# Optimization experiments

Hardware: AMD Instinct MI355X
Metric: run time of the kernel (lower is better)

Reference implementation:

```python
import jax, jax.numpy as jnp
import numpy as np

NUM_OBJ = 3
MIN_OBJ_SCALE = 0.1
MAX_OBJ_SCALE = 0.8
MIN_Y_SCALE = 0.75
MAX_Y_SCALE = 1.25
OBJ_POS_BOUND = 0.9
EPS_FIX = 0.095
BIG = 1e12


def setup_inputs() -> dict:
    key = jax.random.key(0)
    k1, k2, k3 = jax.random.split(key, 3)
    n, T, C, H, W = 64, 32, 3, 64, 64
    x = jax.random.normal(k1, (n, T, C, H, W), dtype=jnp.float32)
    d = C * H * W
    W_enc = jax.random.normal(k2, (d, NUM_OBJ * 8), dtype=jnp.float32) / np.sqrt(d).astype(np.float32)
    b_enc = jax.random.normal(k3, (NUM_OBJ * 8,), dtype=jnp.float32) * 0.01
    return {"x": x, "W_enc": W_enc, "b_enc": b_enc}


def _constrain_zp_mean(zp):
    # zp: (nTo, 8) -> mean (nTo, 4). std branch is discarded by forward().
    zm = jnp.concatenate([jax.nn.sigmoid(zp[:, 0:2]), 2.0 * jax.nn.sigmoid(zp[:, 2:4]) - 1.0], -1)
    set_max = jnp.array([[MAX_OBJ_SCALE - MIN_OBJ_SCALE, MAX_Y_SCALE - MIN_Y_SCALE, OBJ_POS_BOUND, OBJ_POS_BOUND]], dtype=zp.dtype)
    set_min = jnp.array([[MIN_OBJ_SCALE, MIN_Y_SCALE, 0.0, 0.0]], dtype=zp.dtype)
    return zm * set_max + set_min


def _greedy_assign(errors):
    # errors: (n, o, o). Greedy row-by-row argmin, masking out used columns with BIG,
    # exactly as the torch fault-fix loop does via scatter of 1e12.
    n, o, _ = errors.shape
    def step(used, i):
        e = errors[:, i, :] + used * BIG
        j = jnp.argmin(e, -1)
        used = used + jax.nn.one_hot(j, o, dtype=errors.dtype)
        return used, j
    _, js = jax.lax.scan(step, jnp.zeros((n, o), errors.dtype), jnp.arange(o))
    return jnp.moveaxis(js, 0, 1)  # (n, o)


def _match_objects(z):
    # z: (n, T, o, 4). Sequential greedy matching over time.
    def step(prev, z_t):
        curr = jax.lax.stop_gradient(z_t[:, :, 2:4])          # (n, o, 2)
        prv = jax.lax.stop_gradient(prev[:, :, 2:4])          # (n, o, 2)
        errors = jnp.sum((prv[:, :, None, :] - curr[:, None, :, :]) ** 2, -1)  # (n, i, j)
        idx = jnp.argmin(errors, -1)                          # (n, o)
        # fault = assignment is not a permutation (num_obj==3 check from source)
        ok = jnp.all(idx[:, 1:] != idx[:, :-1], -1) & (idx[:, 0] != idx[:, 2])
        gidx = _greedy_assign(errors)
        idx = jnp.where(ok[:, None], idx, gidx)
        match = jnp.take_along_axis(z_t, idx[:, :, None], axis=1)
        return match, match
    z0 = z[:, 0]
    _, rest = jax.lax.scan(step, z0, jnp.moveaxis(z[:, 1:], 1, 0))
    return jnp.concatenate([z0[:, None], jnp.moveaxis(rest, 0, 1)], 1)


def _fix_supair(z):
    # z: (n, T, o, 4). Replace isolated position jumps with neighbor average.
    n, T, o, d = z.shape
    diffs = jax.lax.stop_gradient(jnp.abs(z[:, 1:, :, :2] - z[:, :-1, :, :2]))
    zpad2 = jnp.zeros((n, 1, o, 2), z.dtype)
    prev = jnp.concatenate([zpad2, diffs], 1)
    after = jnp.concatenate([diffs, zpad2], 1)
    mask = (prev > EPS_FIX) & (after > EPS_FIX)               # (n, T, o, 2)
    zpad = jnp.zeros((n, 1, o, d), z.dtype)
    smooth = jnp.concatenate([zpad, (z[:, :-2] + z[:, 2:]) / 2, zpad], 1)
    mask_full = jnp.concatenate((d // 2) * [mask], -1)        # (n, T, o, 4)
    return jnp.where(mask_full, smooth, z)


def reference(x, W_enc, b_enc):
    n, T = x.shape[0], x.shape[1]
    # encoder: per-frame linear to (num_obj, 8) z-parameters
    zp = x.reshape(n * T, -1) @ W_enc + b_enc                  # (nT, o*8)
    zm = _constrain_zp_mean(zp.reshape(-1, 8))                 # (nTo, 4)
    z = zm.reshape(n, T, NUM_OBJ, 4)
    z = _match_objects(z)
    z = _fix_supair(z)
    # v_from_state
    v = z[:, 1:, :, 2:] - z[:, :-1, :, 2:]
    zf = jnp.concatenate([z[:, 1:], v], -1)                    # (n, T-1, o, 6)
    zf = jnp.concatenate([jnp.zeros_like(zf[:, 0:1]), zf], 1)  # (n, T, o, 6)
    zf = zf[:, 1:, :, 2:]                                      # (n, T-1, o, 4)
    zf = jnp.concatenate([(zf[..., :2] + 1) / 2 * 10, zf[..., 2:] / 2 * 10], -1)
    zf = jnp.concatenate([zf[..., :2] / 5, zf[..., 2:] * 2], -1)
    return zf
```

## Files before the change

kernel.cpp:

```cpp
#include <hip/hip_runtime.h>

#define N_B   64
#define T_S   32
#define DIM   12288
#define ROWS  2048
#define NCOL  12
#define RPB   4
#define KSPL  4
#define KSEG  (DIM / KSPL)
#define TILE  1024
#define NTILE (KSEG / TILE)

typedef float f4 __attribute__((ext_vector_type(4)));

__global__ __launch_bounds__(256) void k_tw(const float* __restrict__ W,
                                            float* __restrict__ Wt) {
    const int idx = blockIdx.x * 256 + threadIdx.x;
    const int c   = idx / DIM;
    const int k   = idx - c * DIM;
    const int cm  = ((c >> 2) << 3) | (c & 3);
    Wt[idx] = W[k * 24 + cm];
}

__global__ __launch_bounds__(256) void k_gemm(const float* __restrict__ x,
                                              const float* __restrict__ Wt,
                                              float* __restrict__ part) {
    const int rb  = blockIdx.x >> 2;
    const int sg  = blockIdx.x & 3;
    const int r0  = rb * RPB;
    const int k00 = sg * KSEG;
    const int tid = threadIdx.x;

    float acc[RPB][NCOL];
#pragma unroll
    for (int r = 0; r < RPB; ++r)
#pragma unroll
        for (int c = 0; c < NCOL; ++c) acc[r][c] = 0.f;

#pragma unroll
    for (int t = 0; t < NTILE; ++t) {
        const int kb = k00 + t * TILE + tid * 4;
        f4 wv[NCOL];
#pragma unroll
        for (int c = 0; c < NCOL; ++c)
            wv[c] = *(const f4*)(Wt + (size_t)c * DIM + kb);
        f4 xv[RPB];
#pragma unroll
        for (int r = 0; r < RPB; ++r)
            xv[r] = __builtin_nontemporal_load(
                        (const f4*)(x + (size_t)(r0 + r) * DIM + kb));
#pragma unroll
        for (int r = 0; r < RPB; ++r)
#pragma unroll
            for (int c = 0; c < NCOL; ++c)
                acc[r][c] += xv[r][0] * wv[c][0] + xv[r][1] * wv[c][1] +
                             xv[r][2] * wv[c][2] + xv[r][3] * wv[c][3];
    }

#pragma unroll
    for (int r = 0; r < RPB; ++r)
#pragma unroll
        for (int c = 0; c < NCOL; ++c) {
            float v = acc[r][c];
            v += __shfl_xor(v, 32, 64);
            v += __shfl_xor(v, 16, 64);
            v += __shfl_xor(v, 8, 64);
            v += __shfl_xor(v, 4, 64);
            v += __shfl_xor(v, 2, 64);
            v += __shfl_xor(v, 1, 64);
            acc[r][c] = v;
        }

    __shared__ float red[4][RPB * NCOL];
    const int wave = tid >> 6;
    const int lane = tid & 63;
    if (lane == 0) {
#pragma unroll
        for (int r = 0; r < RPB; ++r)
#pragma unroll
            for (int c = 0; c < NCOL; ++c)
                red[wave][r * NCOL + c] = acc[r][c];
    }
    __syncthreads();

    if (tid < RPB * NCOL) {
        const float s = red[0][tid] + red[1][tid] + red[2][tid] + red[3][tid];
        part[(size_t)sg * (ROWS * NCOL) + (size_t)r0 * NCOL + tid] = s;
    }
}

__global__ __launch_bounds__(256) void k_reduce(const float* __restrict__ part,
                                                const float* __restrict__ b_enc,
                                                float* __restrict__ zbuf) {
    const int rc = blockIdx.x * 256 + threadIdx.x;
    float s = part[rc] + part[ROWS * NCOL + rc] +
              part[2 * ROWS * NCOL + rc] + part[3 * ROWS * NCOL + rc];

    const int c  = rc % NCOL;
    const int o  = c >> 2;
    const int cp = c & 3;
    s += b_enc[o * 8 + cp];
    const float sg = 1.f / (1.f + expf(-s));
    float v;
    if (cp == 0)      v = sg * 0.7f + 0.1f;
    else if (cp == 1) v = sg * 0.5f + 0.75f;
    else              v = (2.f * sg - 1.f) * 0.9f;
    zbuf[rc] = v;
}

__global__ __launch_bounds__(64) void k_post(const float* __restrict__ zbuf,
                                             float* __restrict__ out) {
    __shared__ float z[T_S * NCOL];
    __shared__ float zm[T_S * NCOL];
    __shared__ float zf[T_S * NCOL];
    __shared__ int   perm[T_S];
    const int b   = blockIdx.x;
    const int tid = threadIdx.x;

#pragma unroll
    for (int i = 0; i < 6; ++i)
        z[tid + 64 * i] = zbuf[b * 384 + tid + 64 * i];
    __syncthreads();

    if (tid == 0) {
        float px0 = z[2],  py0 = z[3];
        float px1 = z[6],  py1 = z[7];
        float px2 = z[10], py2 = z[11];
        for (int t = 1; t < T_S; ++t) {
            const int base = t * 12;
            const float cx0 = z[base + 2],  cy0 = z[base + 3];
            const float cx1 = z[base + 6],  cy1 = z[base + 7];
            const float cx2 = z[base + 10], cy2 = z[base + 11];

            float dx, dy;
            dx = px0 - cx0; dy = py0 - cy0; const float e00 = dx * dx + dy * dy;
            dx = px0 - cx1; dy = py0 - cy1; const float e01 = dx * dx + dy * dy;
            dx = px0 - cx2; dy = py0 - cy2; const float e02 = dx * dx + dy * dy;
            dx = px1 - cx0; dy = py1 - cy0; const float e10 = dx * dx + dy * dy;
            dx = px1 - cx1; dy = py1 - cy1; const float e11 = dx * dx + dy * dy;
            dx = px1 - cx2; dy = py1 - cy2; const float e12 = dx * dx + dy * dy;
            dx = px2 - cx0; dy = py2 - cy0; const float e20 = dx * dx + dy * dy;
            dx = px2 - cx1; dy = py2 - cy1; const float e21 = dx * dx + dy * dy;
            dx = px2 - cx2; dy = py2 - cy2; const float e22 = dx * dx + dy * dy;

            auto amin3 = [](float a0, float a1, float a2) {
                int j = 0; float e = a0;
                if (a1 < e) { e = a1; j = 1; }
                if (a2 < e) { j = 2; }
                return j;
            };
            int i0 = amin3(e00, e01, e02);
            int i1 = amin3(e10, e11, e12);
            int i2 = amin3(e20, e21, e22);
            const bool ok = (i1 != i0) && (i2 != i1) && (i0 != i2);
            if (!ok) {
                float u0 = 0.f, u1 = 0.f, u2 = 0.f;
                i0 = amin3(e00, e01, e02);
                if (i0 == 0) u0 = 1.f; else if (i0 == 1) u1 = 1.f; else u2 = 1.f;
                i1 = amin3(e10 + u0 * 1e12f, e11 + u1 * 1e12f, e12 + u2 * 1e12f);
                if (i1 == 0) u0 = 1.f; else if (i1 == 1) u1 = 1.f; else u2 = 1.f;
                i2 = amin3(e20 + u0 * 1e12f, e21 + u1 * 1e12f, e22 + u2 * 1e12f);
            }
            perm[t] = i0 * 9 + i1 * 3 + i2;
            px0 = (i0 == 0) ? cx0 : (i0 == 1) ? cx1 : cx2;
            py0 = (i0 == 0) ? cy0 : (i0 == 1) ? cy1 : cy2;
            px1 = (i1 == 0) ? cx0 : (i1 == 1) ? cx1 : cx2;
            py1 = (i1 == 0) ? cy0 : (i1 == 1) ? cy1 : cy2;
            px2 = (i2 == 0) ? cx0 : (i2 == 1) ? cx1 : cx2;
            py2 = (i2 == 0) ? cy0 : (i2 == 1) ? cy1 : cy2;
        }
    }
    __syncthreads();

#pragma unroll
    for (int ii = 0; ii < 6; ++ii) {
        const int i  = tid + 64 * ii;
        const int t  = i / 12;
        const int j  = i - t * 12;
        const int k  = j >> 2;
        const int ch = j & 3;
        int p = k;
        if (t > 0) {
            const int code = perm[t];
            p = (k == 0) ? code / 9 : (k == 1) ? (code % 9) / 3 : code % 3;
        }
        zm[i] = z[t * 12 + p * 4 + ch];
    }
    __syncthreads();

#pragma unroll
    for (int ii = 0; ii < 6; ++ii) {
        const int i  = tid + 64 * ii;
        const int t  = i / 12;
        const int j  = i - t * 12;
        const int o  = j >> 2;
        const int cc = j & 1;
        const int mb = o * 4 + cc;
        const float pd = (t >= 1)  ? fabsf(zm[t * 12 + mb] - zm[(t - 1) * 12 + mb]) : 0.f;
        const float ad = (t <= 30) ? fabsf(zm[(t + 1) * 12 + mb] - zm[t * 12 + mb]) : 0.f;
        const bool  m  = (pd > 0.095f) && (ad > 0.095f);
        const float sm = (t >= 1 && t <= 30)
                             ? (zm[(t - 1) * 12 + j] + zm[(t + 1) * 12 + j]) * 0.5f
                             : 0.f;
        zf[i] = m ? sm : zm[t * 12 + j];
    }
    __syncthreads();

    for (int i = tid; i < 31 * 12; i += 64) {
        const int t  = i / 12;
        const int j  = i - t * 12;
        const int o  = j >> 2;
        const int c2 = j & 3;
        const int pb = o * 4 + 2 + (c2 & 1);
        float v;
        if (c2 < 2) v = zf[(t + 1) * 12 + pb] + 1.f;
        else        v = (zf[(t + 1) * 12 + pb] - zf[t * 12 + pb]) * 10.f;
        out[b * 372 + i] = v;
    }
}

extern "C" void kernel_launch(void* const* d_in, const int* in_sizes, int n_in,
                              void* d_out, int out_size, void* d_ws, size_t ws_size,
                              hipStream_t stream) {
    (void)in_sizes; (void)n_in; (void)out_size; (void)ws_size;
    const float* x     = (const float*)d_in[0];
    const float* W_enc = (const float*)d_in[1];
    const float* b_enc = (const float*)d_in[2];
    float* out  = (float*)d_out;

    float* zbuf = (float*)d_ws;
    float* Wt   = zbuf + ROWS * NCOL;
    float* part = Wt + NCOL * DIM;

    k_tw    <<<(NCOL * DIM) / 256, 256, 0, stream>>>(W_enc, Wt);
    k_gemm  <<<(ROWS / RPB) * KSPL, 256, 0, stream>>>(x, Wt, part);
    k_reduce<<<(ROWS * NCOL) / 256, 256, 0, stream>>>(part, b_enc, zbuf);
    k_post  <<<N_B, 64, 0, stream>>>(zbuf, out);
}
```

Baseline: 180.0 us.

## Give each wave its own rows in GEMM and split K eight ways

The encoder GEMM now assigns four rows to each wave, so a block covers 16 rows, and each wave walks its own K segment in a rolled loop. The K dimension is split into 8 segments instead of 4, and the reduce kernel sums all of them. The intent is to reuse each W load across more rows per block (fewer loads of W per x byte), drop the cross-wave shared-memory reduction and change the grid shape. It also removes the nontemporal hint on the x loads and writes twice as many partial sums.

```diff
diff --git a/kernel.cpp b/kernel.cpp
--- a/kernel.cpp
+++ b/kernel.cpp
@@ -5,13 +5,10 @@
 #define DIM   12288
 #define ROWS  2048
 #define NCOL  12
-#define RPB   4
-#define KSPL  4
+#define RPB   16
+#define KSPL  8
 #define KSEG  (DIM / KSPL)
-#define TILE  1024
-#define NTILE (KSEG / TILE)
-
-typedef float f4 __attribute__((ext_vector_type(4)));
+#define JSTEP (KSEG / 256)
 
 __global__ __launch_bounds__(256) void k_tw(const float* __restrict__ W,
                                             float* __restrict__ Wt) {
@@ -25,40 +22,41 @@
 __global__ __launch_bounds__(256) void k_gemm(const float* __restrict__ x,
                                               const float* __restrict__ Wt,
                                               float* __restrict__ part) {
-    const int rb  = blockIdx.x >> 2;
-    const int sg  = blockIdx.x & 3;
-    const int r0  = rb * RPB;
-    const int k00 = sg * KSEG;
-    const int tid = threadIdx.x;
-
-    float acc[RPB][NCOL];
-#pragma unroll
-    for (int r = 0; r < RPB; ++r)
+    const int rb   = blockIdx.x >> 3;
+    const int sg   = blockIdx.x & 7;
+    const int tid  = threadIdx.x;
+    const int wave = tid >> 6;
+    const int lane = tid & 63;
+    const int r0   = rb * RPB + wave * 4;
+    const int kb0  = sg * KSEG + lane * 4;
+
+    float acc[4][NCOL];
+#pragma unroll
+    for (int r = 0; r < 4; ++r)
 #pragma unroll
         for (int c = 0; c < NCOL; ++c) acc[r][c] = 0.f;
 
-#pragma unroll
-    for (int t = 0; t < NTILE; ++t) {
-        const int kb = k00 + t * TILE + tid * 4;
-        f4 wv[NCOL];
+#pragma unroll 1
+    for (int j = 0; j < JSTEP; ++j) {
+        const int kb = kb0 + j * 256;
+        float4 wv[NCOL];
 #pragma unroll
         for (int c = 0; c < NCOL; ++c)
-            wv[c] = *(const f4*)(Wt + (size_t)c * DIM + kb);
-        f4 xv[RPB];
-#pragma unroll
-        for (int r = 0; r < RPB; ++r)
-            xv[r] = __builtin_nontemporal_load(
-                        (const f4*)(x + (size_t)(r0 + r) * DIM + kb));
-#pragma unroll
-        for (int r = 0; r < RPB; ++r)
+            wv[c] = *(const float4*)(Wt + (size_t)c * DIM + kb);
+        float4 xv[4];
+#pragma unroll
+        for (int r = 0; r < 4; ++r)
+            xv[r] = *(const float4*)(x + (size_t)(r0 + r) * DIM + kb);
+#pragma unroll
+        for (int r = 0; r < 4; ++r)
 #pragma unroll
             for (int c = 0; c < NCOL; ++c)
-                acc[r][c] += xv[r][0] * wv[c][0] + xv[r][1] * wv[c][1] +
-                             xv[r][2] * wv[c][2] + xv[r][3] * wv[c][3];
-    }
-
-#pragma unroll
-    for (int r = 0; r < RPB; ++r)
+                acc[r][c] += xv[r].x * wv[c].x + xv[r].y * wv[c].y +
+                             xv[r].z * wv[c].z + xv[r].w * wv[c].w;
+    }
+
+#pragma unroll
+    for (int r = 0; r < 4; ++r)
 #pragma unroll
         for (int c = 0; c < NCOL; ++c) {
             float v = acc[r][c];
@@ -71,30 +69,27 @@
             acc[r][c] = v;
         }
 
-    __shared__ float red[4][RPB * NCOL];
-    const int wave = tid >> 6;
-    const int lane = tid & 63;
+    __shared__ float red[RPB * NCOL];
     if (lane == 0) {
 #pragma unroll
-        for (int r = 0; r < RPB; ++r)
+        for (int r = 0; r < 4; ++r)
 #pragma unroll
             for (int c = 0; c < NCOL; ++c)
-                red[wave][r * NCOL + c] = acc[r][c];
-    }
-    __syncthreads();
-
-    if (tid < RPB * NCOL) {
-        const float s = red[0][tid] + red[1][tid] + red[2][tid] + red[3][tid];
-        part[(size_t)sg * (ROWS * NCOL) + (size_t)r0 * NCOL + tid] = s;
-    }
+                red[(wave * 4 + r) * NCOL + c] = acc[r][c];
+    }
+    __syncthreads();
+
+    if (tid < RPB * NCOL)
+        part[(size_t)sg * (ROWS * NCOL) + (size_t)rb * (RPB * NCOL) + tid] = red[tid];
 }
 
 __global__ __launch_bounds__(256) void k_reduce(const float* __restrict__ part,
                                                 const float* __restrict__ b_enc,
                                                 float* __restrict__ zbuf) {
     const int rc = blockIdx.x * 256 + threadIdx.x;
-    float s = part[rc] + part[ROWS * NCOL + rc] +
-              part[2 * ROWS * NCOL + rc] + part[3 * ROWS * NCOL + rc];
+    float s = 0.f;
+#pragma unroll
+    for (int i = 0; i < KSPL; ++i) s += part[(size_t)i * (ROWS * NCOL) + rc];
 
     const int c  = rc % NCOL;
     const int o  = c >> 2;
```

Result: faster. 174.1 us (-3.3%).
